# Performance work log

Hardware: AMD Instinct MI355X
Metric: run time of the kernel (lower is better)

Reference implementation:

```python
import jax, jax.numpy as jnp
import numpy as np

N = 50000
E = 800000
IN_CH = 256
HID = 32
HEADS = 4
OUT_CH = 40
NEG_SLOPE = 0.2
BN_EPS = 1e-5


def _gat_conv(x, W, att_src, att_dst, bias, src, dst, num_nodes, concat):
    # x: [N, F_in]; W: [F_in, H*C]; att_src/att_dst: [H, C]
    H, C = att_src.shape
    h = (x @ W).reshape(num_nodes, H, C)            # [N, H, C]
    a_src = (h * att_src[None]).sum(-1)             # [N, H]
    a_dst = (h * att_dst[None]).sum(-1)             # [N, H]
    e = jax.nn.leaky_relu(a_src[src] + a_dst[dst], NEG_SLOPE)  # [Etot, H]
    # segment softmax over incoming edges of each destination node
    m = jax.ops.segment_max(e, dst, num_segments=num_nodes)    # [N, H]
    ex = jnp.exp(e - m[dst])
    s = jax.ops.segment_sum(ex, dst, num_segments=num_nodes)   # [N, H]
    alpha = ex / (s[dst] + 1e-16)                   # [Etot, H]
    out = jax.ops.segment_sum(h[src] * alpha[:, :, None], dst,
                              num_segments=num_nodes)          # [N, H, C]
    out = out.reshape(num_nodes, H * C) if concat else out.mean(axis=1)
    return out + bias


def setup_inputs() -> dict:
    key = jax.random.key(0)
    ks = jax.random.split(key, 12)
    x = jax.random.normal(ks[0], (N, IN_CH), dtype=jnp.float32)
    edge_index = jax.random.randint(ks[1], (2, E), 0, N, dtype=jnp.int64)
    # layer 1: in -> heads*hid, concat
    W1 = jax.random.normal(ks[2], (IN_CH, HEADS * HID), dtype=jnp.float32) * (1.0 / np.sqrt(IN_CH))
    att_src1 = jax.random.normal(ks[3], (HEADS, HID), dtype=jnp.float32) * 0.1
    att_dst1 = jax.random.normal(ks[4], (HEADS, HID), dtype=jnp.float32) * 0.1
    b1 = jnp.zeros((HEADS * HID,), dtype=jnp.float32)
    # batch norm over hidden*heads features
    gamma = jnp.ones((HEADS * HID,), dtype=jnp.float32)
    beta = jnp.zeros((HEADS * HID,), dtype=jnp.float32)
    # layer 2: heads*hid -> out, heads=1, mean (concat=False)
    W2 = jax.random.normal(ks[5], (HEADS * HID, OUT_CH), dtype=jnp.float32) * (1.0 / np.sqrt(HEADS * HID))
    att_src2 = jax.random.normal(ks[6], (1, OUT_CH), dtype=jnp.float32) * 0.1
    att_dst2 = jax.random.normal(ks[7], (1, OUT_CH), dtype=jnp.float32) * 0.1
    b2 = jnp.zeros((OUT_CH,), dtype=jnp.float32)
    return {"x": x, "edge_index": edge_index, "W1": W1, "att_src1": att_src1,
            "att_dst1": att_dst1, "b1": b1, "gamma": gamma, "beta": beta,
            "W2": W2, "att_src2": att_src2, "att_dst2": att_dst2, "b2": b2}


def reference(x, edge_index, W1, att_src1, att_dst1, b1, gamma, beta,
              W2, att_src2, att_dst2, b2):
    num_nodes = x.shape[0]
    loops = jnp.arange(num_nodes, dtype=edge_index.dtype)
    src = jnp.concatenate([edge_index[0], loops])   # add self-loops (PyG default)
    dst = jnp.concatenate([edge_index[1], loops])
    h = _gat_conv(x, W1, att_src1, att_dst1, b1, src, dst, num_nodes, concat=True)
    # BatchNorm over nodes (training-mode batch statistics)
    mu = h.mean(axis=0)
    var = h.var(axis=0)
    h = (h - mu) * jax.lax.rsqrt(var + BN_EPS) * gamma + beta
    h = jax.nn.elu(h)
    out = _gat_conv(h, W2, att_src2, att_dst2, b2, src, dst, num_nodes, concat=False)
    return out
```

## Files before the change

### kernel.cpp

```cpp
#include <hip/hip_runtime.h>

#define NN 50000
#define EE 800000
#define ETOT 850000
#define FIN 256
#define F1 128
#define F2 40
#define CAP 48
#define G1B ((NN + 127) / 128)
#define FILLB ((EE / 4 + NN + 255) / 256)

typedef unsigned int u32;
typedef unsigned short u16;

static __device__ __forceinline__ u32 f2bf(float f) {
  u32 u = __float_as_uint(f);
  return (u + 0x7FFFu + ((u >> 16) & 1u)) >> 16;
}
#define BF_LO(u) __uint_as_float((u) << 16)
#define BF_HI(u) __uint_as_float((u) & 0xFFFF0000u)

__global__ __launch_bounds__(256) void g1f_kernel(const float* __restrict__ x,
                                                  const float* __restrict__ W1,
                                                  const float* __restrict__ att_src,
                                                  const float* __restrict__ att_dst,
                                                  u32* __restrict__ h1bf,
                                                  float* __restrict__ a_src,
                                                  float* __restrict__ a_dst,
                                                  const int* __restrict__ ei,
                                                  int* __restrict__ cnt,
                                                  int* __restrict__ csr) {
  __shared__ float Alds[16 * 132];
  __shared__ float Blds[16 * 128];
  __shared__ float att_s[128], att_d[128];
  const int t = threadIdx.x;

  if (blockIdx.x >= G1B) {
    int i = (blockIdx.x - G1B) * 256 + t;
    if (i < EE / 4) {
      int e = i * 4;
      int4 s4 = *(const int4*)(ei + e);
      int4 d4 = *(const int4*)(ei + EE + e);
      int p0 = atomicAdd(cnt + d4.x, 1); if (p0 < CAP) csr[d4.x * CAP + p0] = s4.x;
      int p1 = atomicAdd(cnt + d4.y, 1); if (p1 < CAP) csr[d4.y * CAP + p1] = s4.y;
      int p2 = atomicAdd(cnt + d4.z, 1); if (p2 < CAP) csr[d4.z * CAP + p2] = s4.z;
      int p3 = atomicAdd(cnt + d4.w, 1); if (p3 < CAP) csr[d4.w * CAP + p3] = s4.w;
    } else {
      int n = i - EE / 4;
      if (n < NN) {
        int p = atomicAdd(cnt + n, 1);
        if (p < CAP) csr[n * CAP + p] = n;
      }
    }
    return;
  }

  if (t < 128) { att_s[t] = att_src[t]; att_d[t] = att_dst[t]; }
  const int m0 = blockIdx.x * 128;
  const int arow = t >> 1;
  const int akk = (t & 1) * 8;
  const int brow = t >> 4;
  const int bc = (t & 15) * 8;
  const int ty = t >> 4;
  const int tx = t & 15;

  float acc[8][8];
#pragma unroll
  for (int i = 0; i < 8; ++i)
#pragma unroll
    for (int j = 0; j < 8; ++j) acc[i][j] = 0.f;

  for (int k0 = 0; k0 < FIN; k0 += 16) {
    float4 a0 = {0.f, 0.f, 0.f, 0.f}, a1 = {0.f, 0.f, 0.f, 0.f};
    int gr = m0 + arow;
    if (gr < NN) {
      a0 = *(const float4*)(x + (size_t)gr * FIN + k0 + akk);
      a1 = *(const float4*)(x + (size_t)gr * FIN + k0 + akk + 4);
    }
    float4 b0 = *(const float4*)(W1 + (size_t)(k0 + brow) * F1 + bc);
    float4 b1 = *(const float4*)(W1 + (size_t)(k0 + brow) * F1 + bc + 4);
    __syncthreads();
    Alds[(akk + 0) * 132 + arow] = a0.x;
    Alds[(akk + 1) * 132 + arow] = a0.y;
    Alds[(akk + 2) * 132 + arow] = a0.z;
    Alds[(akk + 3) * 132 + arow] = a0.w;
    Alds[(akk + 4) * 132 + arow] = a1.x;
    Alds[(akk + 5) * 132 + arow] = a1.y;
    Alds[(akk + 6) * 132 + arow] = a1.z;
    Alds[(akk + 7) * 132 + arow] = a1.w;
    *(float4*)(Blds + brow * 128 + bc) = b0;
    *(float4*)(Blds + brow * 128 + bc + 4) = b1;
    __syncthreads();
#pragma unroll
    for (int k = 0; k < 16; ++k) {
      float4 av0 = *(const float4*)(Alds + k * 132 + ty * 8);
      float4 av1 = *(const float4*)(Alds + k * 132 + ty * 8 + 4);
      float4 bv0 = *(const float4*)(Blds + k * 128 + tx * 8);
      float4 bv1 = *(const float4*)(Blds + k * 128 + tx * 8 + 4);
      float aa[8] = {av0.x, av0.y, av0.z, av0.w, av1.x, av1.y, av1.z, av1.w};
      float bb[8] = {bv0.x, bv0.y, bv0.z, bv0.w, bv1.x, bv1.y, bv1.z, bv1.w};
#pragma unroll
      for (int i = 0; i < 8; ++i)
#pragma unroll
        for (int j = 0; j < 8; ++j) acc[i][j] = fmaf(aa[i], bb[j], acc[i][j]);
    }
  }
#pragma unroll
  for (int i = 0; i < 8; ++i) {
    int gr = m0 + ty * 8 + i;
    if (gr < NN) {
      uint4 w;
      w.x = f2bf(acc[i][0]) | (f2bf(acc[i][1]) << 16);
      w.y = f2bf(acc[i][2]) | (f2bf(acc[i][3]) << 16);
      w.z = f2bf(acc[i][4]) | (f2bf(acc[i][5]) << 16);
      w.w = f2bf(acc[i][6]) | (f2bf(acc[i][7]) << 16);
      *(uint4*)(h1bf + (size_t)gr * 64 + tx * 4) = w;
    }
  }
#pragma unroll
  for (int i = 0; i < 8; ++i) {
    float ps = 0.f, pd = 0.f;
#pragma unroll
    for (int j = 0; j < 8; ++j) {
      int c = tx * 8 + j;
      ps += acc[i][j] * att_s[c];
      pd += acc[i][j] * att_d[c];
    }
    ps += __shfl_xor(ps, 1); pd += __shfl_xor(pd, 1);
    ps += __shfl_xor(ps, 2); pd += __shfl_xor(pd, 2);
    if ((tx & 3) == 0) {
      int gr = m0 + ty * 8 + i;
      if (gr < NN) {
        int head = tx >> 2;
        a_src[gr * 4 + head] = ps;
        a_dst[gr * 4 + head] = pd;
      }
    }
  }
}

__global__ __launch_bounds__(256) void gather1_kernel(const int* __restrict__ cnt,
                                                      const int* __restrict__ csr,
                                                      const float* __restrict__ a_src,
                                                      const float* __restrict__ a_dst,
                                                      const u32* __restrict__ h1bf,
                                                      const float* __restrict__ b1,
                                                      float* __restrict__ h1b,
                                                      float* __restrict__ bnsum,
                                                      float* __restrict__ bnsq) {
  __shared__ float bns[128], bnq[128];
  int t = threadIdx.x;
  if (t < 128) { bns[t] = 0.f; bnq[t] = 0.f; }
  __syncthreads();
  int n = blockIdx.x * 16 + (t >> 4);
  int l = t & 15;
  int head = l >> 2;
  int f0 = l * 8;
  float adst = a_dst[n * 4 + head];
  float acc[8] = {0.f, 0.f, 0.f, 0.f, 0.f, 0.f, 0.f, 0.f};
  float ssum = 0.f;
  const int* row = csr + n * CAP;
  int m = cnt[n]; if (m > CAP) m = CAP;
  int i = 0;
  for (; i + 3 < m; i += 4) {
    int4 s4 = *(const int4*)(row + i);
    float e0 = a_src[s4.x * 4 + head] + adst;
    float e1 = a_src[s4.y * 4 + head] + adst;
    float e2 = a_src[s4.z * 4 + head] + adst;
    float e3 = a_src[s4.w * 4 + head] + adst;
    uint4 q0 = *(const uint4*)(h1bf + (size_t)s4.x * 64 + l * 4);
    uint4 q1 = *(const uint4*)(h1bf + (size_t)s4.y * 64 + l * 4);
    uint4 q2 = *(const uint4*)(h1bf + (size_t)s4.z * 64 + l * 4);
    uint4 q3 = *(const uint4*)(h1bf + (size_t)s4.w * 64 + l * 4);
    e0 = e0 > 0.f ? e0 : 0.2f * e0;  float x0 = __expf(e0);
    e1 = e1 > 0.f ? e1 : 0.2f * e1;  float x1 = __expf(e1);
    e2 = e2 > 0.f ? e2 : 0.2f * e2;  float x2 = __expf(e2);
    e3 = e3 > 0.f ? e3 : 0.2f * e3;  float x3 = __expf(e3);
    acc[0] = fmaf(x0, BF_LO(q0.x), acc[0]); acc[1] = fmaf(x0, BF_HI(q0.x), acc[1]);
    acc[2] = fmaf(x0, BF_LO(q0.y), acc[2]); acc[3] = fmaf(x0, BF_HI(q0.y), acc[3]);
    acc[4] = fmaf(x0, BF_LO(q0.z), acc[4]); acc[5] = fmaf(x0, BF_HI(q0.z), acc[5]);
    acc[6] = fmaf(x0, BF_LO(q0.w), acc[6]); acc[7] = fmaf(x0, BF_HI(q0.w), acc[7]);
    acc[0] = fmaf(x1, BF_LO(q1.x), acc[0]); acc[1] = fmaf(x1, BF_HI(q1.x), acc[1]);
    acc[2] = fmaf(x1, BF_LO(q1.y), acc[2]); acc[3] = fmaf(x1, BF_HI(q1.y), acc[3]);
    acc[4] = fmaf(x1, BF_LO(q1.z), acc[4]); acc[5] = fmaf(x1, BF_HI(q1.z), acc[5]);
    acc[6] = fmaf(x1, BF_LO(q1.w), acc[6]); acc[7] = fmaf(x1, BF_HI(q1.w), acc[7]);
    acc[0] = fmaf(x2, BF_LO(q2.x), acc[0]); acc[1] = fmaf(x2, BF_HI(q2.x), acc[1]);
    acc[2] = fmaf(x2, BF_LO(q2.y), acc[2]); acc[3] = fmaf(x2, BF_HI(q2.y), acc[3]);
    acc[4] = fmaf(x2, BF_LO(q2.z), acc[4]); acc[5] = fmaf(x2, BF_HI(q2.z), acc[5]);
    acc[6] = fmaf(x2, BF_LO(q2.w), acc[6]); acc[7] = fmaf(x2, BF_HI(q2.w), acc[7]);
    acc[0] = fmaf(x3, BF_LO(q3.x), acc[0]); acc[1] = fmaf(x3, BF_HI(q3.x), acc[1]);
    acc[2] = fmaf(x3, BF_LO(q3.y), acc[2]); acc[3] = fmaf(x3, BF_HI(q3.y), acc[3]);
    acc[4] = fmaf(x3, BF_LO(q3.z), acc[4]); acc[5] = fmaf(x3, BF_HI(q3.z), acc[5]);
    acc[6] = fmaf(x3, BF_LO(q3.w), acc[6]); acc[7] = fmaf(x3, BF_HI(q3.w), acc[7]);
    ssum += x0 + x1 + x2 + x3;
  }
  for (; i < m; ++i) {
    int s0 = row[i];
    float e0 = a_src[s0 * 4 + head] + adst;
    e0 = e0 > 0.f ? e0 : 0.2f * e0;
    float x0 = __expf(e0);
    uint4 q = *(const uint4*)(h1bf + (size_t)s0 * 64 + l * 4);
    acc[0] = fmaf(x0, BF_LO(q.x), acc[0]); acc[1] = fmaf(x0, BF_HI(q.x), acc[1]);
    acc[2] = fmaf(x0, BF_LO(q.y), acc[2]); acc[3] = fmaf(x0, BF_HI(q.y), acc[3]);
    acc[4] = fmaf(x0, BF_LO(q.z), acc[4]); acc[5] = fmaf(x0, BF_HI(q.z), acc[5]);
    acc[6] = fmaf(x0, BF_LO(q.w), acc[6]); acc[7] = fmaf(x0, BF_HI(q.w), acc[7]);
    ssum += x0;
  }
  float inv = 1.f / (ssum + 1e-16f);
  float4 b0 = *(const float4*)(b1 + f0);
  float4 b4 = *(const float4*)(b1 + f0 + 4);
  float o[8];
  o[0] = acc[0] * inv + b0.x; o[1] = acc[1] * inv + b0.y;
  o[2] = acc[2] * inv + b0.z; o[3] = acc[3] * inv + b0.w;
  o[4] = acc[4] * inv + b4.x; o[5] = acc[5] * inv + b4.y;
  o[6] = acc[6] * inv + b4.z; o[7] = acc[7] * inv + b4.w;
  float4 w0 = {o[0], o[1], o[2], o[3]};
  float4 w1 = {o[4], o[5], o[6], o[7]};
  *(float4*)(h1b + (size_t)n * F1 + f0) = w0;
  *(float4*)(h1b + (size_t)n * F1 + f0 + 4) = w1;
#pragma unroll
  for (int j = 0; j < 8; ++j) {
    atomicAdd(&bns[f0 + j], o[j]);
    atomicAdd(&bnq[f0 + j], o[j] * o[j]);
  }
  __syncthreads();
  if (t < 128) {
    atomicAdd(bnsum + t, bns[t]);
    atomicAdd(bnsq + t, bnq[t]);
  }
}

__global__ __launch_bounds__(256) void gemm2_kernel(const float* __restrict__ hpre,
                                                    const float* __restrict__ W2,
                                                    const float* __restrict__ bnsum,
                                                    const float* __restrict__ bnsq,
                                                    const float* __restrict__ gamma,
                                                    const float* __restrict__ beta,
                                                    const float* __restrict__ att_src2,
                                                    const float* __restrict__ att_dst2,
                                                    u16* __restrict__ h2bf,
                                                    float* __restrict__ a_src2,
                                                    float* __restrict__ a_dst2) {
  __shared__ float Wlds[128 * 40];
  __shared__ float Alds[16 * 128];
  __shared__ float sc[128], sh[128];
  int t = threadIdx.x;
  for (int i = t; i < 128 * 40; i += 256) Wlds[i] = W2[i];
  if (t < 128) {
    const float invN = 1.f / (float)NN;
    float mu = bnsum[t] * invN;
    float var = bnsq[t] * invN - mu * mu;
    float s = gamma[t] * rsqrtf(var + 1e-5f);
    sc[t] = s;
    sh[t] = beta[t] - mu * s;
  }
  int tr = t >> 3;
  int tc = t & 7;
  float as5[5], ad5[5];
#pragma unroll
  for (int j = 0; j < 5; ++j) { as5[j] = att_src2[tc * 5 + j]; ad5[j] = att_dst2[tc * 5 + j]; }
  int n0 = blockIdx.x * 128;
  int lrow = t >> 1;
  int lkk = (t & 1) * 8;
  float acc[4][5];
#pragma unroll
  for (int i = 0; i < 4; ++i)
#pragma unroll
    for (int j = 0; j < 5; ++j) acc[i][j] = 0.f;

  for (int k0 = 0; k0 < F1; k0 += 16) {
    float av[8];
    int gn = n0 + lrow;
    if (gn < NN) {
      float4 v0 = *(const float4*)(hpre + (size_t)gn * F1 + k0 + lkk);
      float4 v1 = *(const float4*)(hpre + (size_t)gn * F1 + k0 + lkk + 4);
      av[0] = v0.x; av[1] = v0.y; av[2] = v0.z; av[3] = v0.w;
      av[4] = v1.x; av[5] = v1.y; av[6] = v1.z; av[7] = v1.w;
    } else {
#pragma unroll
      for (int j = 0; j < 8; ++j) av[j] = 0.f;
    }
    __syncthreads();
#pragma unroll
    for (int j = 0; j < 8; ++j) {
      int kg = k0 + lkk + j;
      float a = av[j] * sc[kg] + sh[kg];
      a = a > 0.f ? a : (__expf(a) - 1.f);
      Alds[(lkk + j) * 128 + lrow] = a;
    }
    __syncthreads();
#pragma unroll
    for (int k = 0; k < 16; ++k) {
      float4 a4 = *(const float4*)(Alds + k * 128 + tr * 4);
      float aa[4] = {a4.x, a4.y, a4.z, a4.w};
      float w[5];
#pragma unroll
      for (int j = 0; j < 5; ++j) w[j] = Wlds[(k0 + k) * 40 + tc * 5 + j];
#pragma unroll
      for (int i = 0; i < 4; ++i)
#pragma unroll
        for (int j = 0; j < 5; ++j) acc[i][j] = fmaf(aa[i], w[j], acc[i][j]);
    }
  }
#pragma unroll
  for (int i = 0; i < 4; ++i) {
    int gn = n0 + tr * 4 + i;
    if (gn < NN) {
#pragma unroll
      for (int j = 0; j < 5; ++j)
        h2bf[(size_t)gn * 40 + tc * 5 + j] = (u16)f2bf(acc[i][j]);
    }
  }
#pragma unroll
  for (int i = 0; i < 4; ++i) {
    float ps = 0.f, pd = 0.f;
#pragma unroll
    for (int j = 0; j < 5; ++j) { ps += acc[i][j] * as5[j]; pd += acc[i][j] * ad5[j]; }
#pragma unroll
    for (int off = 1; off < 8; off <<= 1) {
      ps += __shfl_xor(ps, off);
      pd += __shfl_xor(pd, off);
    }
    if (tc == 0) {
      int gn = n0 + tr * 4 + i;
      if (gn < NN) { a_src2[gn] = ps; a_dst2[gn] = pd; }
    }
  }
}

__global__ __launch_bounds__(256) void gather2_kernel(const int* __restrict__ cnt,
                                                      const int* __restrict__ csr,
                                                      const float* __restrict__ a_src,
                                                      const float* __restrict__ a_dst,
                                                      const u32* __restrict__ h2bf,
                                                      const float* __restrict__ b2,
                                                      float* __restrict__ out) {
  int t = threadIdx.x;
  int n = blockIdx.x * 32 + (t >> 3);
  if (n >= NN) return;
  int l = t & 7;
  bool act = (l < 5);
  float adst = a_dst[n];
  float acc[8] = {0.f, 0.f, 0.f, 0.f, 0.f, 0.f, 0.f, 0.f};
  float ssum = 0.f;
  const int* row = csr + n * CAP;
  int m = cnt[n]; if (m > CAP) m = CAP;
  const uint4 zz = {0u, 0u, 0u, 0u};
  int i = 0;
  for (; i + 3 < m; i += 4) {
    int4 s4 = *(const int4*)(row + i);
    float e0 = a_src[s4.x] + adst;
    float e1 = a_src[s4.y] + adst;
    float e2 = a_src[s4.z] + adst;
    float e3 = a_src[s4.w] + adst;
    uint4 q0 = act ? *(const uint4*)(h2bf + (size_t)s4.x * 20 + l * 4) : zz;
    uint4 q1 = act ? *(const uint4*)(h2bf + (size_t)s4.y * 20 + l * 4) : zz;
    uint4 q2 = act ? *(const uint4*)(h2bf + (size_t)s4.z * 20 + l * 4) : zz;
    uint4 q3 = act ? *(const uint4*)(h2bf + (size_t)s4.w * 20 + l * 4) : zz;
    e0 = e0 > 0.f ? e0 : 0.2f * e0;  float x0 = __expf(e0);
    e1 = e1 > 0.f ? e1 : 0.2f * e1;  float x1 = __expf(e1);
    e2 = e2 > 0.f ? e2 : 0.2f * e2;  float x2 = __expf(e2);
    e3 = e3 > 0.f ? e3 : 0.2f * e3;  float x3 = __expf(e3);
    acc[0] = fmaf(x0, BF_LO(q0.x), acc[0]); acc[1] = fmaf(x0, BF_HI(q0.x), acc[1]);
    acc[2] = fmaf(x0, BF_LO(q0.y), acc[2]); acc[3] = fmaf(x0, BF_HI(q0.y), acc[3]);
    acc[4] = fmaf(x0, BF_LO(q0.z), acc[4]); acc[5] = fmaf(x0, BF_HI(q0.z), acc[5]);
    acc[6] = fmaf(x0, BF_LO(q0.w), acc[6]); acc[7] = fmaf(x0, BF_HI(q0.w), acc[7]);
    acc[0] = fmaf(x1, BF_LO(q1.x), acc[0]); acc[1] = fmaf(x1, BF_HI(q1.x), acc[1]);
    acc[2] = fmaf(x1, BF_LO(q1.y), acc[2]); acc[3] = fmaf(x1, BF_HI(q1.y), acc[3]);
    acc[4] = fmaf(x1, BF_LO(q1.z), acc[4]); acc[5] = fmaf(x1, BF_HI(q1.z), acc[5]);
    acc[6] = fmaf(x1, BF_LO(q1.w), acc[6]); acc[7] = fmaf(x1, BF_HI(q1.w), acc[7]);
    acc[0] = fmaf(x2, BF_LO(q2.x), acc[0]); acc[1] = fmaf(x2, BF_HI(q2.x), acc[1]);
    acc[2] = fmaf(x2, BF_LO(q2.y), acc[2]); acc[3] = fmaf(x2, BF_HI(q2.y), acc[3]);
    acc[4] = fmaf(x2, BF_LO(q2.z), acc[4]); acc[5] = fmaf(x2, BF_HI(q2.z), acc[5]);
    acc[6] = fmaf(x2, BF_LO(q2.w), acc[6]); acc[7] = fmaf(x2, BF_HI(q2.w), acc[7]);
    acc[0] = fmaf(x3, BF_LO(q3.x), acc[0]); acc[1] = fmaf(x3, BF_HI(q3.x), acc[1]);
    acc[2] = fmaf(x3, BF_LO(q3.y), acc[2]); acc[3] = fmaf(x3, BF_HI(q3.y), acc[3]);
    acc[4] = fmaf(x3, BF_LO(q3.z), acc[4]); acc[5] = fmaf(x3, BF_HI(q3.z), acc[5]);
    acc[6] = fmaf(x3, BF_LO(q3.w), acc[6]); acc[7] = fmaf(x3, BF_HI(q3.w), acc[7]);
    ssum += x0 + x1 + x2 + x3;
  }
  for (; i < m; ++i) {
    int s0 = row[i];
    float e0 = a_src[s0] + adst;
    e0 = e0 > 0.f ? e0 : 0.2f * e0;
    float x0 = __expf(e0);
    uint4 q = act ? *(const uint4*)(h2bf + (size_t)s0 * 20 + l * 4) : zz;
    acc[0] = fmaf(x0, BF_LO(q.x), acc[0]); acc[1] = fmaf(x0, BF_HI(q.x), acc[1]);
    acc[2] = fmaf(x0, BF_LO(q.y), acc[2]); acc[3] = fmaf(x0, BF_HI(q.y), acc[3]);
    acc[4] = fmaf(x0, BF_LO(q.z), acc[4]); acc[5] = fmaf(x0, BF_HI(q.z), acc[5]);
    acc[6] = fmaf(x0, BF_LO(q.w), acc[6]); acc[7] = fmaf(x0, BF_HI(q.w), acc[7]);
    ssum += x0;
  }
  float inv = 1.f / (ssum + 1e-16f);
  if (act) {
    float* op = out + (size_t)n * F2 + l * 8;
#pragma unroll
    for (int j = 0; j < 8; ++j) op[j] = acc[j] * inv + b2[l * 8 + j];
  }
}

extern "C" void kernel_launch(void* const* d_in, const int* in_sizes, int n_in,
                              void* d_out, int out_size, void* d_ws, size_t ws_size,
                              hipStream_t stream) {
  const float* x        = (const float*)d_in[0];
  const int*   ei       = (const int*)d_in[1];
  const float* W1       = (const float*)d_in[2];
  const float* att_src1 = (const float*)d_in[3];
  const float* att_dst1 = (const float*)d_in[4];
  const float* b1       = (const float*)d_in[5];
  const float* gamma    = (const float*)d_in[6];
  const float* beta     = (const float*)d_in[7];
  const float* W2       = (const float*)d_in[8];
  const float* att_src2 = (const float*)d_in[9];
  const float* att_dst2 = (const float*)d_in[10];
  const float* b2       = (const float*)d_in[11];
  float* out = (float*)d_out;

  int* cnt      = (int*)d_ws;
  float* bnsum  = (float*)(cnt + 50048);
  float* bnsq   = bnsum + 128;
  int* csr      = (int*)(bnsq + 128);
  u32* h1bf     = (u32*)(csr + NN * CAP);
  float* h1b    = (float*)(h1bf + 3200000);
  u32* h2bf     = (u32*)(h1b + 6400000);
  float* a_src1 = (float*)(h2bf + 1000000);
  float* a_dst1 = a_src1 + 200000;
  float* a_src2 = a_dst1 + 200000;
  float* a_dst2 = a_src2 + 50000;

  hipMemsetAsync(cnt, 0, (50048 + 256) * sizeof(int), stream);

  g1f_kernel<<<G1B + FILLB, 256, 0, stream>>>(x, W1, att_src1, att_dst1,
                                              h1bf, a_src1, a_dst1,
                                              ei, cnt, csr);
  gather1_kernel<<<NN / 16, 256, 0, stream>>>(cnt, csr, a_src1, a_dst1,
                                              h1bf, b1, h1b, bnsum, bnsq);
  gemm2_kernel<<<(NN + 127) / 128, 256, 0, stream>>>(h1b, W2, bnsum, bnsq,
                                                     gamma, beta,
                                                     att_src2, att_dst2,
                                                     (u16*)h2bf, a_src2, a_dst2);
  gather2_kernel<<<(NN + 31) / 32, 256, 0, stream>>>(cnt, csr, a_src2, a_dst2,
                                                     h2bf, b2, out);
}
```

Measured before the change: 329.7 us.

## Split layer-1 gather by head so each block handles one head's slice

The layer-1 aggregation kernel now launches four groups of blocks, one per attention head. Each thread group of four lanes handles one node's 32-feature head slice instead of sixteen lanes covering all 128 features. This shrinks each block's working set of gathered h1 rows to 64 bytes per source node, which may improve L2 hit rates across blocks running the same head. The trade-off is that the CSR rows, counts and a_dst are each read four times, and the per-block batch-norm partials go through LDS atomics on a smaller 32-entry array.

```diff
diff --git a/kernel.cpp b/kernel.cpp
--- a/kernel.cpp
+++ b/kernel.cpp
@@ -9,6 +9,7 @@
 #define CAP 48
 #define G1B ((NN + 127) / 128)
 #define FILLB ((EE / 4 + NN + 255) / 256)
+#define PB ((NN + 63) / 64)
 
 typedef unsigned int u32;
 typedef unsigned short u16;
@@ -148,85 +149,90 @@
                                                       float* __restrict__ h1b,
                                                       float* __restrict__ bnsum,
                                                       float* __restrict__ bnsq) {
-  __shared__ float bns[128], bnq[128];
+  __shared__ float bns[32], bnq[32];
   int t = threadIdx.x;
-  if (t < 128) { bns[t] = 0.f; bnq[t] = 0.f; }
+  if (t < 32) { bns[t] = 0.f; bnq[t] = 0.f; }
   __syncthreads();
-  int n = blockIdx.x * 16 + (t >> 4);
-  int l = t & 15;
-  int head = l >> 2;
-  int f0 = l * 8;
-  float adst = a_dst[n * 4 + head];
-  float acc[8] = {0.f, 0.f, 0.f, 0.f, 0.f, 0.f, 0.f, 0.f};
-  float ssum = 0.f;
-  const int* row = csr + n * CAP;
-  int m = cnt[n]; if (m > CAP) m = CAP;
-  int i = 0;
-  for (; i + 3 < m; i += 4) {
-    int4 s4 = *(const int4*)(row + i);
-    float e0 = a_src[s4.x * 4 + head] + adst;
-    float e1 = a_src[s4.y * 4 + head] + adst;
-    float e2 = a_src[s4.z * 4 + head] + adst;
-    float e3 = a_src[s4.w * 4 + head] + adst;
-    uint4 q0 = *(const uint4*)(h1bf + (size_t)s4.x * 64 + l * 4);
-    uint4 q1 = *(const uint4*)(h1bf + (size_t)s4.y * 64 + l * 4);
-    uint4 q2 = *(const uint4*)(h1bf + (size_t)s4.z * 64 + l * 4);
-    uint4 q3 = *(const uint4*)(h1bf + (size_t)s4.w * 64 + l * 4);
-    e0 = e0 > 0.f ? e0 : 0.2f * e0;  float x0 = __expf(e0);
-    e1 = e1 > 0.f ? e1 : 0.2f * e1;  float x1 = __expf(e1);
-    e2 = e2 > 0.f ? e2 : 0.2f * e2;  float x2 = __expf(e2);
-    e3 = e3 > 0.f ? e3 : 0.2f * e3;  float x3 = __expf(e3);
-    acc[0] = fmaf(x0, BF_LO(q0.x), acc[0]); acc[1] = fmaf(x0, BF_HI(q0.x), acc[1]);
-    acc[2] = fmaf(x0, BF_LO(q0.y), acc[2]); acc[3] = fmaf(x0, BF_HI(q0.y), acc[3]);
-    acc[4] = fmaf(x0, BF_LO(q0.z), acc[4]); acc[5] = fmaf(x0, BF_HI(q0.z), acc[5]);
-    acc[6] = fmaf(x0, BF_LO(q0.w), acc[6]); acc[7] = fmaf(x0, BF_HI(q0.w), acc[7]);
-    acc[0] = fmaf(x1, BF_LO(q1.x), acc[0]); acc[1] = fmaf(x1, BF_HI(q1.x), acc[1]);
-    acc[2] = fmaf(x1, BF_LO(q1.y), acc[2]); acc[3] = fmaf(x1, BF_HI(q1.y), acc[3]);
-    acc[4] = fmaf(x1, BF_LO(q1.z), acc[4]); acc[5] = fmaf(x1, BF_HI(q1.z), acc[5]);
-    acc[6] = fmaf(x1, BF_LO(q1.w), acc[6]); acc[7] = fmaf(x1, BF_HI(q1.w), acc[7]);
-    acc[0] = fmaf(x2, BF_LO(q2.x), acc[0]); acc[1] = fmaf(x2, BF_HI(q2.x), acc[1]);
-    acc[2] = fmaf(x2, BF_LO(q2.y), acc[2]); acc[3] = fmaf(x2, BF_HI(q2.y), acc[3]);
-    acc[4] = fmaf(x2, BF_LO(q2.z), acc[4]); acc[5] = fmaf(x2, BF_HI(q2.z), acc[5]);
-    acc[6] = fmaf(x2, BF_LO(q2.w), acc[6]); acc[7] = fmaf(x2, BF_HI(q2.w), acc[7]);
-    acc[0] = fmaf(x3, BF_LO(q3.x), acc[0]); acc[1] = fmaf(x3, BF_HI(q3.x), acc[1]);
-    acc[2] = fmaf(x3, BF_LO(q3.y), acc[2]); acc[3] = fmaf(x3, BF_HI(q3.y), acc[3]);
-    acc[4] = fmaf(x3, BF_LO(q3.z), acc[4]); acc[5] = fmaf(x3, BF_HI(q3.z), acc[5]);
-    acc[6] = fmaf(x3, BF_LO(q3.w), acc[6]); acc[7] = fmaf(x3, BF_HI(q3.w), acc[7]);
-    ssum += x0 + x1 + x2 + x3;
-  }
-  for (; i < m; ++i) {
-    int s0 = row[i];
-    float e0 = a_src[s0 * 4 + head] + adst;
-    e0 = e0 > 0.f ? e0 : 0.2f * e0;
-    float x0 = __expf(e0);
-    uint4 q = *(const uint4*)(h1bf + (size_t)s0 * 64 + l * 4);
-    acc[0] = fmaf(x0, BF_LO(q.x), acc[0]); acc[1] = fmaf(x0, BF_HI(q.x), acc[1]);
-    acc[2] = fmaf(x0, BF_LO(q.y), acc[2]); acc[3] = fmaf(x0, BF_HI(q.y), acc[3]);
-    acc[4] = fmaf(x0, BF_LO(q.z), acc[4]); acc[5] = fmaf(x0, BF_HI(q.z), acc[5]);
-    acc[6] = fmaf(x0, BF_LO(q.w), acc[6]); acc[7] = fmaf(x0, BF_HI(q.w), acc[7]);
-    ssum += x0;
-  }
-  float inv = 1.f / (ssum + 1e-16f);
-  float4 b0 = *(const float4*)(b1 + f0);
-  float4 b4 = *(const float4*)(b1 + f0 + 4);
-  float o[8];
-  o[0] = acc[0] * inv + b0.x; o[1] = acc[1] * inv + b0.y;
-  o[2] = acc[2] * inv + b0.z; o[3] = acc[3] * inv + b0.w;
-  o[4] = acc[4] * inv + b4.x; o[5] = acc[5] * inv + b4.y;
-  o[6] = acc[6] * inv + b4.z; o[7] = acc[7] * inv + b4.w;
-  float4 w0 = {o[0], o[1], o[2], o[3]};
-  float4 w1 = {o[4], o[5], o[6], o[7]};
-  *(float4*)(h1b + (size_t)n * F1 + f0) = w0;
-  *(float4*)(h1b + (size_t)n * F1 + f0 + 4) = w1;
-#pragma unroll
-  for (int j = 0; j < 8; ++j) {
-    atomicAdd(&bns[f0 + j], o[j]);
-    atomicAdd(&bnq[f0 + j], o[j] * o[j]);
+  int p = blockIdx.x / PB;
+  int nb = blockIdx.x - p * PB;
+  int n = nb * 64 + (t >> 2);
+  int l = t & 3;
+  int f0 = p * 32 + l * 8;
+  if (n < NN) {
+    float adst = a_dst[n * 4 + p];
+    float acc[8] = {0.f, 0.f, 0.f, 0.f, 0.f, 0.f, 0.f, 0.f};
+    float ssum = 0.f;
+    const int* row = csr + n * CAP;
+    int m = cnt[n]; if (m > CAP) m = CAP;
+    const u32* hb = h1bf + p * 16 + l * 4;
+    int i = 0;
+    for (; i + 3 < m; i += 4) {
+      int4 s4 = *(const int4*)(row + i);
+      float e0 = a_src[s4.x * 4 + p] + adst;
+      float e1 = a_src[s4.y * 4 + p] + adst;
+      float e2 = a_src[s4.z * 4 + p] + adst;
+      float e3 = a_src[s4.w * 4 + p] + adst;
+      uint4 q0 = *(const uint4*)(hb + (size_t)s4.x * 64);
+      uint4 q1 = *(const uint4*)(hb + (size_t)s4.y * 64);
+      uint4 q2 = *(const uint4*)(hb + (size_t)s4.z * 64);
+      uint4 q3 = *(const uint4*)(hb + (size_t)s4.w * 64);
+      e0 = e0 > 0.f ? e0 : 0.2f * e0;  float x0 = __expf(e0);
+      e1 = e1 > 0.f ? e1 : 0.2f * e1;  float x1 = __expf(e1);
+      e2 = e2 > 0.f ? e2 : 0.2f * e2;  float x2 = __expf(e2);
+      e3 = e3 > 0.f ? e3 : 0.2f * e3;  float x3 = __expf(e3);
+      acc[0] = fmaf(x0, BF_LO(q0.x), acc[0]); acc[1] = fmaf(x0, BF_HI(q0.x), acc[1]);
+      acc[2] = fmaf(x0, BF_LO(q0.y), acc[2]); acc[3] = fmaf(x0, BF_HI(q0.y), acc[3]);
+      acc[4] = fmaf(x0, BF_LO(q0.z), acc[4]); acc[5] = fmaf(x0, BF_HI(q0.z), acc[5]);
+      acc[6] = fmaf(x0, BF_LO(q0.w), acc[6]); acc[7] = fmaf(x0, BF_HI(q0.w), acc[7]);
+      acc[0] = fmaf(x1, BF_LO(q1.x), acc[0]); acc[1] = fmaf(x1, BF_HI(q1.x), acc[1]);
+      acc[2] = fmaf(x1, BF_LO(q1.y), acc[2]); acc[3] = fmaf(x1, BF_HI(q1.y), acc[3]);
+      acc[4] = fmaf(x1, BF_LO(q1.z), acc[4]); acc[5] = fmaf(x1, BF_HI(q1.z), acc[5]);
+      acc[6] = fmaf(x1, BF_LO(q1.w), acc[6]); acc[7] = fmaf(x1, BF_HI(q1.w), acc[7]);
+      acc[0] = fmaf(x2, BF_LO(q2.x), acc[0]); acc[1] = fmaf(x2, BF_HI(q2.x), acc[1]);
+      acc[2] = fmaf(x2, BF_LO(q2.y), acc[2]); acc[3] = fmaf(x2, BF_HI(q2.y), acc[3]);
+      acc[4] = fmaf(x2, BF_LO(q2.z), acc[4]); acc[5] = fmaf(x2, BF_HI(q2.z), acc[5]);
+      acc[6] = fmaf(x2, BF_LO(q2.w), acc[6]); acc[7] = fmaf(x2, BF_HI(q2.w), acc[7]);
+      acc[0] = fmaf(x3, BF_LO(q3.x), acc[0]); acc[1] = fmaf(x3, BF_HI(q3.x), acc[1]);
+      acc[2] = fmaf(x3, BF_LO(q3.y), acc[2]); acc[3] = fmaf(x3, BF_HI(q3.y), acc[3]);
+      acc[4] = fmaf(x3, BF_LO(q3.z), acc[4]); acc[5] = fmaf(x3, BF_HI(q3.z), acc[5]);
+      acc[6] = fmaf(x3, BF_LO(q3.w), acc[6]); acc[7] = fmaf(x3, BF_HI(q3.w), acc[7]);
+      ssum += x0 + x1 + x2 + x3;
+    }
+    for (; i < m; ++i) {
+      int s0 = row[i];
+      float e0 = a_src[s0 * 4 + p] + adst;
+      e0 = e0 > 0.f ? e0 : 0.2f * e0;
+      float x0 = __expf(e0);
+      uint4 q = *(const uint4*)(hb + (size_t)s0 * 64);
+      acc[0] = fmaf(x0, BF_LO(q.x), acc[0]); acc[1] = fmaf(x0, BF_HI(q.x), acc[1]);
+      acc[2] = fmaf(x0, BF_LO(q.y), acc[2]); acc[3] = fmaf(x0, BF_HI(q.y), acc[3]);
+      acc[4] = fmaf(x0, BF_LO(q.z), acc[4]); acc[5] = fmaf(x0, BF_HI(q.z), acc[5]);
+      acc[6] = fmaf(x0, BF_LO(q.w), acc[6]); acc[7] = fmaf(x0, BF_HI(q.w), acc[7]);
+      ssum += x0;
+    }
+    float inv = 1.f / (ssum + 1e-16f);
+    float4 b0 = *(const float4*)(b1 + f0);
+    float4 b4 = *(const float4*)(b1 + f0 + 4);
+    float o[8];
+    o[0] = acc[0] * inv + b0.x; o[1] = acc[1] * inv + b0.y;
+    o[2] = acc[2] * inv + b0.z; o[3] = acc[3] * inv + b0.w;
+    o[4] = acc[4] * inv + b4.x; o[5] = acc[5] * inv + b4.y;
+    o[6] = acc[6] * inv + b4.z; o[7] = acc[7] * inv + b4.w;
+    float4 w0 = {o[0], o[1], o[2], o[3]};
+    float4 w1 = {o[4], o[5], o[6], o[7]};
+    *(float4*)(h1b + (size_t)n * F1 + f0) = w0;
+    *(float4*)(h1b + (size_t)n * F1 + f0 + 4) = w1;
+    int lb = l * 8;
+#pragma unroll
+    for (int j = 0; j < 8; ++j) {
+      atomicAdd(&bns[lb + j], o[j]);
+      atomicAdd(&bnq[lb + j], o[j] * o[j]);
+    }
   }
   __syncthreads();
-  if (t < 128) {
-    atomicAdd(bnsum + t, bns[t]);
-    atomicAdd(bnsq + t, bnq[t]);
+  if (t < 32) {
+    atomicAdd(bnsum + p * 32 + t, bns[t]);
+    atomicAdd(bnsq + p * 32 + t, bnq[t]);
   }
 }
 
@@ -433,8 +439,8 @@
   g1f_kernel<<<G1B + FILLB, 256, 0, stream>>>(x, W1, att_src1, att_dst1,
                                               h1bf, a_src1, a_dst1,
                                               ei, cnt, csr);
-  gather1_kernel<<<NN / 16, 256, 0, stream>>>(cnt, csr, a_src1, a_dst1,
-                                              h1bf, b1, h1b, bnsum, bnsq);
+  gather1_kernel<<<4 * PB, 256, 0, stream>>>(cnt, csr, a_src1, a_dst1,
+                                             h1bf, b1, h1b, bnsum, bnsq);
   gemm2_kernel<<<(NN + 127) / 128, 256, 0, stream>>>(h1b, W2, bnsum, bnsq,
                                                      gamma, beta,
                                                      att_src2, att_dst2,
```

New measurement: 323.8 us. Within noise of the previous version (-1.8%).
